# Kernel optimization log

Hardware: AMD Instinct MI355X
Metric: run time of the kernel (lower is better)

Reference implementation:

```python
import jax, jax.numpy as jnp
import numpy as np

N = 200000       # n_nodes
D = 128          # memory_dimension
E = 100000       # number of unique event source nodes this batch
OUTPUT = 30.0    # time-decay constant for embeddings
LAMB = 1.0 * OUTPUT  # self.lamb = lamb * output, used by memory updater
SLOPE = 0.01     # LeakyReLU default negative slope
EPS = 1e-10


def _leaky(x):
    return jnp.where(x >= 0, x, SLOPE * x)


def setup_inputs() -> dict:
    key = jax.random.key(0)
    ks = jax.random.split(key, 10)
    # memory: [N, D+1]; first D cols = exp-weighted message sum, last col = decayed event count (>=1)
    memory = jax.random.uniform(ks[0], (N, D + 1), dtype=jnp.float32)
    memory = memory.at[:, D].add(1.0)
    last_update = jax.random.uniform(ks[1], (N,), dtype=jnp.float32) * 50.0
    # unique sources (aggregator guarantees uniqueness) -> use a random permutation prefix
    unique_sources = jax.random.permutation(ks[2], N)[:E].astype(jnp.int32)
    unique_messages = jax.random.normal(ks[3], (E, D + 1), dtype=jnp.float32) * 0.1
    unique_messages = unique_messages.at[:, D].set(1.0)  # one event per message (ones column)
    # event times after last_update, before now_time
    unique_timestamps = jax.random.uniform(ks[4], (E,), dtype=jnp.float32) * 50.0 + 50.0
    now_time = jnp.float32(110.0)
    static_emb = jax.random.normal(ks[5], (N, D), dtype=jnp.float32) * 0.1
    W1 = jax.random.normal(ks[6], (2 * D, D), dtype=jnp.float32) / np.sqrt(2 * D)
    b1 = jnp.zeros((D,), dtype=jnp.float32)
    W2 = jax.random.normal(ks[7], (D, D), dtype=jnp.float32) / np.sqrt(D)
    b2 = jnp.zeros((D,), dtype=jnp.float32)
    e_lamb = jnp.float32(0.5)
    return {"memory": memory, "last_update": last_update, "unique_messages": unique_messages,
            "unique_timestamps": unique_timestamps, "static_emb": static_emb,
            "W1": W1, "b1": b1, "W2": W2, "b2": b2, "e_lamb": e_lamb,
            "now_time": now_time, "unique_sources": unique_sources}


def reference(memory, last_update, unique_messages, unique_timestamps, static_emb,
              W1, b1, W2, b2, e_lamb, now_time, unique_sources):
    # --- ExpMemoryUpdater.get_updated_memory: exp-decay old state, add new messages, bump last_update
    decay = jnp.exp((last_update[unique_sources] - unique_timestamps) / LAMB)  # [E]
    new_rows = memory[unique_sources] * decay[:, None] + unique_messages       # [E, D+1]
    upd_mem = memory.at[unique_sources].set(new_rows)                          # [N, D+1]
    upd_lu = last_update.at[unique_sources].set(unique_timestamps)             # [N]
    # --- ExpLambsEmbedding over all nodes: [sum/count, sum] -> cat -> [N, 2D]
    msum = upd_mem[:, :D]
    cnt = upd_mem[:, D:D + 1]
    feat = jnp.concatenate([msum / (cnt + EPS), msum], axis=-1)                # [N, 2D]
    # --- embedding_transform: Linear(2D->D) + LeakyReLU + Linear(D->D) + LeakyReLU
    h = _leaky(_leaky(feat @ W1 + b1) @ W2 + b2)                               # [N, D]
    # --- exponential time-decay to 'now'
    dec = h * jnp.exp((upd_lu - now_time) / OUTPUT)[:, None]                   # [N, D]
    # --- learned convex combination with static embedding table
    return e_lamb * static_emb + (1.0 - e_lamb) * dec
```

## Files before the change

### kernel.cpp

```cpp
#include <hip/hip_runtime.h>
#include <hip/hip_bf16.h>

#define N_ROWS 200000
#define DIMS   128
#define E_UPD  100000
#define TILE   64
#define NTILES (N_ROWS / TILE)
#define FSTRIDE 264
#define HSTRIDE 136
#define MAIN_GRID 768

typedef float f32x4 __attribute__((ext_vector_type(4)));
typedef __bf16 bf16x8 __attribute__((ext_vector_type(8)));
typedef unsigned short u16x8 __attribute__((ext_vector_type(8)));

static __device__ __forceinline__ unsigned short f2b(float f) {
    __hip_bfloat16 b = __float2bfloat16(f);
    return __builtin_bit_cast(unsigned short, b);
}

__global__ void fill_inv(int* inv, int* counter) {
    int i = blockIdx.x * blockDim.x + threadIdx.x;
    if (i < N_ROWS) inv[i] = -1;
    if (i == 0) counter[0] = 0;
}

__global__ void scatter_inv(const int* __restrict__ src, int* __restrict__ inv) {
    int e = blockIdx.x * blockDim.x + threadIdx.x;
    if (e < E_UPD) inv[src[e]] = e;
}

__launch_bounds__(512)
__global__ void ctdg_main(
    const float* __restrict__ memory,
    const float* __restrict__ last_update,
    const float* __restrict__ umsg,
    const float* __restrict__ uts,
    const float* __restrict__ semb,
    const float* __restrict__ W1,
    const float* __restrict__ b1,
    const float* __restrict__ W2,
    const float* __restrict__ b2,
    const float* __restrict__ e_lamb_p,
    const float* __restrict__ now_p,
    const int*   __restrict__ inv,
    int*         __restrict__ counter,
    float*       __restrict__ out)
{
    __shared__ __align__(16) unsigned short feat[TILE][FSTRIDE];
    __shared__ __align__(16) unsigned short h1s[TILE][HSTRIDE];
    __shared__ float rdecay[TILE];
    __shared__ float rcinv[TILE];
    __shared__ float rscale[TILE];
    __shared__ int   ridx[TILE];
    __shared__ int   s_tile;

    const int tid  = threadIdx.x;
    const int lane = tid & 63;
    const int wave = tid >> 6;
    const int quad = lane >> 4;
    const int l16  = lane & 15;
    const int wn   = wave * 16;

    u16x8 w1f[8];
    u16x8 w2f[4];
    #pragma unroll
    for (int t = 0; t < 8; ++t) {
        #pragma unroll
        for (int j = 0; j < 8; ++j)
            w1f[t][j] = f2b(W1[(t*32 + quad*8 + j)*128 + wn + l16]);
    }
    #pragma unroll
    for (int t = 0; t < 4; ++t) {
        #pragma unroll
        for (int j = 0; j < 8; ++j)
            w2f[t][j] = f2b(W2[(t*32 + quad*8 + j)*128 + wn + l16]);
    }
    const float b1v   = b1[wn + l16];
    const float b2v   = b2[wn + l16];
    const float el    = e_lamb_p[0];
    const float nowt  = now_p[0];
    const float inv30 = 1.0f / 30.0f;

    for (;;) {
        if (tid == 0) s_tile = atomicAdd(counter, 1);
        __syncthreads();
        const int tile = s_tile;
        if (tile >= NTILES) break;
        const int row0 = tile * TILE;

        if (tid < TILE) {
            const int g = row0 + tid;
            const float lu = last_update[g];
            const int e = inv[g];
            float dec = 1.0f, cnt, lun;
            const float mc = memory[(size_t)g*129 + 128];
            if (e >= 0) {
                const float ts = uts[e];
                dec = __expf((lu - ts) * inv30);
                cnt = fmaf(mc, dec, umsg[(size_t)e*129 + 128]);
                lun = ts;
            } else {
                cnt = mc;
                lun = lu;
            }
            rdecay[tid] = dec;
            rcinv[tid]  = 1.0f / (cnt + 1e-10f);
            rscale[tid] = __expf((lun - nowt) * inv30);
            ridx[tid]   = e;
        }
        __syncthreads();

        {
            const int r = tid >> 3;
            const int s = tid & 7;
            const int g = row0 + r;
            const float d  = rdecay[r];
            const float ci = rcinv[r];
            const int   e  = ridx[r];
            const float* mrow = memory + (size_t)g*129;
            if (e >= 0) {
                const float* grow = umsg + (size_t)e*129;
                #pragma unroll
                for (int j = 0; j < 16; ++j) {
                    const int c = s + j*8;
                    const float ms = fmaf(mrow[c], d, grow[c]);
                    feat[r][c]       = f2b(ms * ci);
                    feat[r][128 + c] = f2b(ms);
                }
            } else {
                #pragma unroll
                for (int j = 0; j < 16; ++j) {
                    const int c = s + j*8;
                    const float ms = mrow[c];
                    feat[r][c]       = f2b(ms * ci);
                    feat[r][128 + c] = f2b(ms);
                }
            }
        }
        __syncthreads();

        #pragma unroll
        for (int mt = 0; mt < 4; ++mt) {
            f32x4 acc = {0.f, 0.f, 0.f, 0.f};
            const int mrow = mt*16 + l16;
            #pragma unroll
            for (int k = 0; k < 8; ++k) {
                u16x8 a = *(const u16x8*)&feat[mrow][k*32 + quad*8];
                acc = __builtin_amdgcn_mfma_f32_16x16x32_bf16(
                        __builtin_bit_cast(bf16x8, a),
                        __builtin_bit_cast(bf16x8, w1f[k]), acc, 0, 0, 0);
            }
            #pragma unroll
            for (int r = 0; r < 4; ++r) {
                float v = acc[r] + b1v;
                v = (v >= 0.f) ? v : 0.01f * v;
                h1s[mt*16 + quad*4 + r][wn + l16] = f2b(v);
            }
        }
        __syncthreads();

        #pragma unroll
        for (int mt = 0; mt < 4; ++mt) {
            f32x4 acc = {0.f, 0.f, 0.f, 0.f};
            const int mrow = mt*16 + l16;
            #pragma unroll
            for (int k = 0; k < 4; ++k) {
                u16x8 a = *(const u16x8*)&h1s[mrow][k*32 + quad*8];
                acc = __builtin_amdgcn_mfma_f32_16x16x32_bf16(
                        __builtin_bit_cast(bf16x8, a),
                        __builtin_bit_cast(bf16x8, w2f[k]), acc, 0, 0, 0);
            }
            #pragma unroll
            for (int r = 0; r < 4; ++r) {
                const int row = mt*16 + quad*4 + r;
                const int g = row0 + row;
                float v = acc[r] + b2v;
                v = (v >= 0.f) ? v : 0.01f * v;
                v *= rscale[row];
                const float sv = semb[(size_t)g*128 + wn + l16];
                out[(size_t)g*128 + wn + l16] = el * sv + (1.0f - el) * v;
            }
        }
        __syncthreads();
    }
}

extern "C" void kernel_launch(void* const* d_in, const int* in_sizes, int n_in,
                              void* d_out, int out_size, void* d_ws, size_t ws_size,
                              hipStream_t stream) {
    const float* memory      = (const float*)d_in[0];
    const float* last_update = (const float*)d_in[1];
    const float* umsg        = (const float*)d_in[2];
    const float* uts         = (const float*)d_in[3];
    const float* semb        = (const float*)d_in[4];
    const float* W1          = (const float*)d_in[5];
    const float* b1          = (const float*)d_in[6];
    const float* W2          = (const float*)d_in[7];
    const float* b2          = (const float*)d_in[8];
    const float* e_lamb      = (const float*)d_in[9];
    const float* nowt        = (const float*)d_in[10];
    const int*   src         = (const int*)d_in[11];

    int* inv     = (int*)d_ws;
    int* counter = inv + N_ROWS;
    float* out   = (float*)d_out;

    fill_inv<<<(N_ROWS + 255) / 256, 256, 0, stream>>>(inv, counter);
    scatter_inv<<<(E_UPD + 255) / 256, 256, 0, stream>>>(src, inv);
    ctdg_main<<<MAIN_GRID, 512, 0, stream>>>(memory, last_update, umsg, uts, semb,
                                             W1, b1, W2, b2, e_lamb, nowt,
                                             inv, counter, out);
}
```

Before: 325.1 us.

## Factor row-wise 1/count out of first GEMM and merge per-row prologue

Instead of building a 2D-wide bf16 feature tile [msum/cnt, msum], the kernel stores only msum in LDS and runs two MFMA accumulations against the top and bottom halves of W1, combining them as cinv*P + Q. This halves LDS feature writes and footprint, and each thread now computes its row's decay itself, removing one barrier and the separate per-row pass. It also raises the grid to 1024 with an occupancy hint of 8 and uses nontemporal stores for the output. Rounding differs slightly because the division by count now happens after the bf16 matmul, and the occupancy hint may force register spills given the weight fragments held in registers.

After: 387.8 us. +19.3%, slower.

```diff
diff --git a/kernel.cpp b/kernel.cpp
--- a/kernel.cpp
+++ b/kernel.cpp
@@ -6,9 +6,9 @@
 #define E_UPD  100000
 #define TILE   64
 #define NTILES (N_ROWS / TILE)
-#define FSTRIDE 264
+#define MSTRIDE 136
 #define HSTRIDE 136
-#define MAIN_GRID 768
+#define MAIN_GRID 1024
 
 typedef float f32x4 __attribute__((ext_vector_type(4)));
 typedef __bf16 bf16x8 __attribute__((ext_vector_type(8)));
@@ -30,7 +30,7 @@
     if (e < E_UPD) inv[src[e]] = e;
 }
 
-__launch_bounds__(512)
+__launch_bounds__(512, 8)
 __global__ void ctdg_main(
     const float* __restrict__ memory,
     const float* __restrict__ last_update,
@@ -47,12 +47,10 @@
     int*         __restrict__ counter,
     float*       __restrict__ out)
 {
-    __shared__ __align__(16) unsigned short feat[TILE][FSTRIDE];
+    __shared__ __align__(16) unsigned short msum_s[TILE][MSTRIDE];
     __shared__ __align__(16) unsigned short h1s[TILE][HSTRIDE];
-    __shared__ float rdecay[TILE];
     __shared__ float rcinv[TILE];
     __shared__ float rscale[TILE];
-    __shared__ int   ridx[TILE];
     __shared__ int   s_tile;
 
     const int tid  = threadIdx.x;
@@ -62,19 +60,18 @@
     const int l16  = lane & 15;
     const int wn   = wave * 16;
 
-    u16x8 w1f[8];
+    u16x8 w1a[4];
+    u16x8 w1b[4];
     u16x8 w2f[4];
-    #pragma unroll
-    for (int t = 0; t < 8; ++t) {
-        #pragma unroll
-        for (int j = 0; j < 8; ++j)
-            w1f[t][j] = f2b(W1[(t*32 + quad*8 + j)*128 + wn + l16]);
-    }
     #pragma unroll
     for (int t = 0; t < 4; ++t) {
         #pragma unroll
-        for (int j = 0; j < 8; ++j)
-            w2f[t][j] = f2b(W2[(t*32 + quad*8 + j)*128 + wn + l16]);
+        for (int j = 0; j < 8; ++j) {
+            const int kr = t*32 + quad*8 + j;
+            w1a[t][j] = f2b(W1[kr*128 + wn + l16]);
+            w1b[t][j] = f2b(W1[(128 + kr)*128 + wn + l16]);
+            w2f[t][j] = f2b(W2[kr*128 + wn + l16]);
+        }
     }
     const float b1v   = b1[wn + l16];
     const float b2v   = b2[wn + l16];
@@ -82,6 +79,9 @@
     const float nowt  = now_p[0];
     const float inv30 = 1.0f / 30.0f;
 
+    const int r = tid >> 3;
+    const int s = tid & 7;
+
     for (;;) {
         if (tid == 0) s_tile = atomicAdd(counter, 1);
         __syncthreads();
@@ -89,52 +89,41 @@
         if (tile >= NTILES) break;
         const int row0 = tile * TILE;
 
-        if (tid < TILE) {
-            const int g = row0 + tid;
+        {
+            const int g = row0 + r;
             const float lu = last_update[g];
-            const int e = inv[g];
-            float dec = 1.0f, cnt, lun;
+            const int   e  = inv[g];
             const float mc = memory[(size_t)g*129 + 128];
+            const float* mrow = memory + (size_t)g*129;
+            float d, cnt, lun;
             if (e >= 0) {
                 const float ts = uts[e];
-                dec = __expf((lu - ts) * inv30);
-                cnt = fmaf(mc, dec, umsg[(size_t)e*129 + 128]);
+                d   = __expf((lu - ts) * inv30);
+                cnt = fmaf(mc, d, umsg[(size_t)e*129 + 128]);
                 lun = ts;
             } else {
-                cnt = mc;
-                lun = lu;
-            }
-            rdecay[tid] = dec;
-            rcinv[tid]  = 1.0f / (cnt + 1e-10f);
-            rscale[tid] = __expf((lun - nowt) * inv30);
-            ridx[tid]   = e;
-        }
-        __syncthreads();
-
-        {
-            const int r = tid >> 3;
-            const int s = tid & 7;
-            const int g = row0 + r;
-            const float d  = rdecay[r];
-            const float ci = rcinv[r];
-            const int   e  = ridx[r];
-            const float* mrow = memory + (size_t)g*129;
+                d = 1.0f; cnt = mc; lun = lu;
+            }
+            if (s == 0) {
+                rcinv[r]  = 1.0f / (cnt + 1e-10f);
+                rscale[r] = __expf((lun - nowt) * inv30);
+            }
             if (e >= 0) {
                 const float* grow = umsg + (size_t)e*129;
                 #pragma unroll
-                for (int j = 0; j < 16; ++j) {
-                    const int c = s + j*8;
-                    const float ms = fmaf(mrow[c], d, grow[c]);
-                    feat[r][c]       = f2b(ms * ci);
-                    feat[r][128 + c] = f2b(ms);
+                for (int j = 0; j < 8; ++j) {
+                    const int c = 2*s + 16*j;
+                    const float m0 = fmaf(mrow[c],   d, grow[c]);
+                    const float m1 = fmaf(mrow[c+1], d, grow[c+1]);
+                    const unsigned pk = (unsigned)f2b(m0) | ((unsigned)f2b(m1) << 16);
+                    *(unsigned*)&msum_s[r][c] = pk;
                 }
             } else {
                 #pragma unroll
-                for (int j = 0; j < 16; ++j) {
-                    const int c = s + j*8;
-                    const float ms = mrow[c];
-                    feat[r][c]       = f2b(ms * ci);
-                    feat[r][128 + c] = f2b(ms);
+                for (int j = 0; j < 8; ++j) {
+                    const int c = 2*s + 16*j;
+                    const unsigned pk = (unsigned)f2b(mrow[c]) | ((unsigned)f2b(mrow[c+1]) << 16);
+                    *(unsigned*)&msum_s[r][c] = pk;
                 }
             }
         }
@@ -142,20 +131,25 @@
 
         #pragma unroll
         for (int mt = 0; mt < 4; ++mt) {
-            f32x4 acc = {0.f, 0.f, 0.f, 0.f};
+            f32x4 aP = {0.f, 0.f, 0.f, 0.f};
+            f32x4 aQ = {0.f, 0.f, 0.f, 0.f};
             const int mrow = mt*16 + l16;
             #pragma unroll
-            for (int k = 0; k < 8; ++k) {
-                u16x8 a = *(const u16x8*)&feat[mrow][k*32 + quad*8];
-                acc = __builtin_amdgcn_mfma_f32_16x16x32_bf16(
+            for (int k = 0; k < 4; ++k) {
+                u16x8 a = *(const u16x8*)&msum_s[mrow][k*32 + quad*8];
+                aP = __builtin_amdgcn_mfma_f32_16x16x32_bf16(
                         __builtin_bit_cast(bf16x8, a),
-                        __builtin_bit_cast(bf16x8, w1f[k]), acc, 0, 0, 0);
-            }
-            #pragma unroll
-            for (int r = 0; r < 4; ++r) {
-                float v = acc[r] + b1v;
+                        __builtin_bit_cast(bf16x8, w1a[k]), aP, 0, 0, 0);
+                aQ = __builtin_amdgcn_mfma_f32_16x16x32_bf16(
+                        __builtin_bit_cast(bf16x8, a),
+                        __builtin_bit_cast(bf16x8, w1b[k]), aQ, 0, 0, 0);
+            }
+            #pragma unroll
+            for (int rr = 0; rr < 4; ++rr) {
+                const int row = mt*16 + quad*4 + rr;
+                float v = fmaf(rcinv[row], aP[rr], aQ[rr]) + b1v;
                 v = (v >= 0.f) ? v : 0.01f * v;
-                h1s[mt*16 + quad*4 + r][wn + l16] = f2b(v);
+                h1s[row][wn + l16] = f2b(v);
             }
         }
         __syncthreads();
@@ -172,14 +166,15 @@
                         __builtin_bit_cast(bf16x8, w2f[k]), acc, 0, 0, 0);
             }
             #pragma unroll
-            for (int r = 0; r < 4; ++r) {
-                const int row = mt*16 + quad*4 + r;
+            for (int rr = 0; rr < 4; ++rr) {
+                const int row = mt*16 + quad*4 + rr;
                 const int g = row0 + row;
-                float v = acc[r] + b2v;
+                float v = acc[rr] + b2v;
                 v = (v >= 0.f) ? v : 0.01f * v;
                 v *= rscale[row];
                 const float sv = semb[(size_t)g*128 + wn + l16];
-                out[(size_t)g*128 + wn + l16] = el * sv + (1.0f - el) * v;
+                const float o  = el * sv + (1.0f - el) * v;
+                __builtin_nontemporal_store(o, &out[(size_t)g*128 + wn + l16]);
             }
         }
         __syncthreads();
```
